# Optimization experiments

Hardware: AMD Instinct MI355X
Metric: run time of the kernel (lower is better)

## Reference

```python
import jax, jax.numpy as jnp
from jax import lax
import numpy as np

B, CIN, H, W = 1, 3, 96, 96
Q = 65536
C = 64
CU = C * 9              # feat_unfold channels
IN_DIM = CU + 2 + 2     # q_feat + rel_coord + rel_cell
HID = 256
OUT = 3
EPS_SHIFT = 1e-6


def setup_inputs():
    key = jax.random.key(0)
    ks = jax.random.split(key, 16)
    inp = jax.random.normal(ks[0], (B, CIN, H, W), jnp.float32)
    coord = jax.random.uniform(ks[1], (B, Q, 2), jnp.float32, -1.0, 1.0)
    cell = jnp.full((B, Q, 2), 2.0 / 256.0, jnp.float32)  # cell size of a 256x256 output grid
    enc_w = jax.random.normal(ks[2], (C, CIN, 3, 3), jnp.float32) * 0.1
    enc_b = jnp.zeros((C,), jnp.float32)
    dims = [IN_DIM, HID, HID, HID, HID, OUT]
    out = {"inp": inp, "coord": coord, "cell": cell, "enc_w": enc_w, "enc_b": enc_b}
    for i in range(5):
        out[f"w{i}"] = jax.random.normal(ks[3 + i], (dims[i], dims[i + 1]), jnp.float32) * (1.0 / np.sqrt(dims[i]))
        out[f"b{i}"] = jnp.zeros((dims[i + 1],), jnp.float32)
    return out


def _unfold3x3(feat):
    # F.unfold(feat, 3, padding=1).reshape(b, c*9, h, w): channel order c-major, kernel row-major
    b, c, h, w = feat.shape
    p = jnp.pad(feat, ((0, 0), (0, 0), (1, 1), (1, 1)))
    pats = jnp.stack([p[:, :, ki:ki + h, kj:kj + w] for ki in range(3) for kj in range(3)], axis=2)
    return pats.reshape(b, c * 9, h, w)


def _nearest_idx(c, n):
    # torch grid_sample nearest, align_corners=False: unnormalize then round-half-even (nearbyint)
    ix = (c + 1.0) * n / 2.0 - 0.5
    return jnp.clip(jnp.round(ix), 0, n - 1).astype(jnp.int32)


def _gather(fmap, iy, ix):
    # fmap [B,C,H,W], iy/ix [B,Q] -> [B,Q,C]
    return jax.vmap(lambda f, y, x: f[:, y, x].T)(fmap, iy, ix)


def _mlp(x, ws, bs):
    for wgt, b in zip(ws[:-1], bs[:-1]):
        x = jax.nn.relu(x @ wgt + b)
    return x @ ws[-1] + bs[-1]


def reference(inp, coord, cell, enc_w, enc_b, w0, b0, w1, b1, w2, b2, w3, b3, w4, b4):
    ws = [w0, w1, w2, w3, w4]
    bs = [b0, b1, b2, b3, b4]
    # encoder: 3x3 conv, SAME padding
    feat = lax.conv_general_dilated(inp, enc_w, (1, 1), 'SAME') + enc_b[None, :, None, None]
    feat = _unfold3x3(feat)                     # [B, C*9, H, W]
    h, w = feat.shape[2], feat.shape[3]
    rx, ry = 1.0 / h, 1.0 / w                   # 2/r/2
    # make_coord pixel centers
    fcy = -1.0 + (2.0 * jnp.arange(h, dtype=jnp.float32) + 1.0) / h   # [H]
    fcx = -1.0 + (2.0 * jnp.arange(w, dtype=jnp.float32) + 1.0) / w   # [W]
    bnd = 1.0 - 1e-6
    rel_cell = cell * jnp.array([h, w], dtype=cell.dtype)             # [B,Q,2]

    preds, areas = [], []
    for vx in (-1.0, 1.0):
        for vy in (-1.0, 1.0):
            c0 = jnp.clip(coord[..., 0] + vx * rx + EPS_SHIFT, -bnd, bnd)
            c1 = jnp.clip(coord[..., 1] + vy * ry + EPS_SHIFT, -bnd, bnd)
            iy = _nearest_idx(c0, h)            # coord[...,0] indexes dim H
            ix = _nearest_idx(c1, w)
            q_feat = _gather(feat, iy, ix)      # [B,Q,CU]
            rel0 = (coord[..., 0] - fcy[iy]) * h
            rel1 = (coord[..., 1] - fcx[ix]) * w
            mlp_in = jnp.concatenate([q_feat, rel0[..., None], rel1[..., None], rel_cell], axis=-1)
            pred = _mlp(mlp_in.reshape(-1, IN_DIM), ws, bs).reshape(coord.shape[0], coord.shape[1], OUT)
            preds.append(pred)
            areas.append(jnp.abs(rel0 * rel1) + 1e-9)

    tot_area = areas[0] + areas[1] + areas[2] + areas[3]
    # local-ensemble diagonal swap
    areas = [areas[3], areas[2], areas[1], areas[0]]
    ret = 0.0
    for pred, area in zip(preds, areas):
        ret = ret + pred * (area / tot_area)[..., None]
    return ret
```

## Files before the change

### kernel.cpp

```cpp
#include <hip/hip_runtime.h>
#include <math.h>

#define NPOS 9216

using half8  = __attribute__((ext_vector_type(8))) _Float16;
using f32x4  = __attribute__((ext_vector_type(4))) float;
using f32x16 = __attribute__((ext_vector_type(16))) float;

#define OFF_FEATT 0u
#define OFF_A0    1229312u
#define OFF_WF32  5947904u
#define OFF_WF4   6341120u
#define OFF_WB    6349312u

#define NB_FEAT 2401
#define NB_PA   768
#define NB_PW4  16
#define NB_PB   576

__global__ __launch_bounds__(256) void setup_kernel(
    const float* __restrict__ inp, const float* __restrict__ enc_w,
    const float* __restrict__ enc_b, const float* __restrict__ w0,
    const float* __restrict__ w1, const float* __restrict__ w2,
    const float* __restrict__ w3, const float* __restrict__ w4,
    _Float16* __restrict__ featT, _Float16* __restrict__ wf32,
    _Float16* __restrict__ wf4, _Float16* __restrict__ wB)
{
    int blk = blockIdx.x;
    const int t = threadIdx.x;

    if (blk < NB_FEAT) {
        int pp = blk * 4 + (t >> 6);
        int c  = t & 63;
        int py = pp / 98, px = pp - py * 98;
        float acc = 0.0f;
        if (py >= 1 && py <= 96 && px >= 1 && px <= 96) {
            int y = py - 1, x = px - 1;
            acc = enc_b[c];
            #pragma unroll
            for (int cin = 0; cin < 3; ++cin) {
                #pragma unroll
                for (int ky = 0; ky < 3; ++ky) {
                    int yy = y + ky - 1;
                    if (yy < 0 || yy >= 96) continue;
                    #pragma unroll
                    for (int kx = 0; kx < 3; ++kx) {
                        int xx = x + kx - 1;
                        if (xx < 0 || xx >= 96) continue;
                        acc = fmaf(inp[cin * NPOS + yy * 96 + xx],
                                   enc_w[c * 27 + cin * 9 + ky * 3 + kx], acc);
                    }
                }
            }
        }
        featT[pp * 64 + c] = (_Float16)acc;
        return;
    }
    blk -= NB_FEAT;
    if (blk < NB_PA) {
        int idx = blk * 256 + t;
        int l = idx >> 16;
        int r = idx & 65535;
        int j    = r & 7;
        int lane = (r >> 3) & 63;
        int nt32 = (r >> 9) & 7;
        int ks   = r >> 12;
        int n = nt32 * 32 + (lane & 31);
        int k = ks * 16 + ((lane >> 5) << 3) + j;
        const float* W = (l == 0) ? w1 : (l == 1) ? w2 : w3;
        wf32[idx] = (_Float16)W[k * 256 + n];
        return;
    }
    blk -= NB_PA;
    if (blk < NB_PW4) {
        int idx = blk * 256 + t;
        int j    = idx & 7;
        int lane = (idx >> 3) & 63;
        int ks   = idx >> 9;
        int n = lane & 15;
        int k = ks * 32 + ((lane >> 4) << 3) + j;
        wf4[idx] = (n < 3) ? (_Float16)w4[k * 3 + n] : (_Float16)0.0f;
        return;
    }
    blk -= NB_PW4;
    {
        int idx = blk * 256 + t;
        int j    = idx & 7;
        int lane = (idx >> 3) & 63;
        int ntB  = (idx >> 9) & 15;
        int ks   = (idx >> 13) & 1;
        int t9   = idx >> 14;
        int c = ks * 32 + ((lane >> 4) << 3) + j;
        int n = ntB * 16 + (lane & 15);
        wB[idx] = (_Float16)w0[(c * 9 + t9) * 256 + n];
    }
}

__global__ __launch_bounds__(256) void a0_mfma(const _Float16* __restrict__ featT,
                                               const _Float16* __restrict__ wB,
                                               const float* __restrict__ b0,
                                               _Float16* __restrict__ A0)
{
    const int lane = threadIdx.x & 63;
    const int tile = blockIdx.x * 4 + (threadIdx.x >> 6);
    const int l15  = lane & 15;
    const int l4   = lane >> 4;
    int r = tile * 16 + l15;
    int y = r / 96, x = r - y * 96;

    f32x4 acc[16];
    #pragma unroll
    for (int nt = 0; nt < 16; ++nt) acc[nt] = (f32x4){0.f, 0.f, 0.f, 0.f};

    #pragma unroll
    for (int t9 = 0; t9 < 9; ++t9) {
        int ki = t9 / 3, kj = t9 - ki * 3;
        const _Float16* ap = featT + ((y + ki) * 98 + (x + kj)) * 64 + l4 * 8;
        #pragma unroll
        for (int ks = 0; ks < 2; ++ks) {
            half8 a = *(const half8*)(ap + ks * 32);
            const _Float16* bp = wB + ((t9 * 2 + ks) * 16 * 64 + lane) * 8;
            #pragma unroll
            for (int nt = 0; nt < 16; ++nt) {
                half8 b = *(const half8*)(bp + nt * 512);
                acc[nt] = __builtin_amdgcn_mfma_f32_16x16x32_f16(a, b, acc[nt], 0, 0, 0);
            }
        }
    }
    int rb = tile * 16 + l4 * 4;
    #pragma unroll
    for (int nt = 0; nt < 16; ++nt) {
        float bb = b0[nt * 16 + l15];
        #pragma unroll
        for (int i = 0; i < 4; ++i)
            A0[(rb + i) * 256 + nt * 16 + l15] = (_Float16)(acc[nt][i] + bb);
    }
}

__device__ __forceinline__ void hidden32(_Float16 (*h)[264],
                                         const _Float16* __restrict__ W,
                                         const float* __restrict__ bias,
                                         int wm, int wn, int lane)
{
    const int l31 = lane & 31;
    const int l5  = lane >> 5;
    f32x16 a00 = {}, a01 = {}, a10 = {}, a11 = {};
    #pragma unroll
    for (int ks = 0; ks < 16; ++ks) {
        half8 Av0 = *(const half8*)&h[wm * 64 + l31][ks * 16 + l5 * 8];
        half8 Av1 = *(const half8*)&h[wm * 64 + 32 + l31][ks * 16 + l5 * 8];
        const _Float16* bp = W + (ks * 8 + wn * 2) * 512 + lane * 8;
        half8 Bv0 = *(const half8*)bp;
        half8 Bv1 = *(const half8*)(bp + 512);
        a00 = __builtin_amdgcn_mfma_f32_32x32x16_f16(Av0, Bv0, a00, 0, 0, 0);
        a01 = __builtin_amdgcn_mfma_f32_32x32x16_f16(Av0, Bv1, a01, 0, 0, 0);
        a10 = __builtin_amdgcn_mfma_f32_32x32x16_f16(Av1, Bv0, a10, 0, 0, 0);
        a11 = __builtin_amdgcn_mfma_f32_32x32x16_f16(Av1, Bv1, a11, 0, 0, 0);
    }
    __syncthreads();
    float bv0 = bias[wn * 64 + l31];
    float bv1 = bias[wn * 64 + 32 + l31];
    #pragma unroll
    for (int reg = 0; reg < 16; ++reg) {
        int rr = (reg & 3) + ((reg >> 2) << 3) + (l5 << 2);
        int r0 = wm * 64 + rr;
        int c0 = wn * 64 + l31;
        h[r0][c0]           = (_Float16)fmaxf(a00[reg] + bv0, 0.0f);
        h[r0][c0 + 32]      = (_Float16)fmaxf(a01[reg] + bv1, 0.0f);
        h[r0 + 32][c0]      = (_Float16)fmaxf(a10[reg] + bv0, 0.0f);
        h[r0 + 32][c0 + 32] = (_Float16)fmaxf(a11[reg] + bv1, 0.0f);
    }
    __syncthreads();
}

__global__ __launch_bounds__(512, 4) void fused_kernel(
    const _Float16* __restrict__ A0, const float* __restrict__ coord,
    const float* __restrict__ cell, const float* __restrict__ w0,
    const float* __restrict__ b1, const float* __restrict__ b2,
    const float* __restrict__ b3, const float* __restrict__ b4,
    const _Float16* __restrict__ wf32, const _Float16* __restrict__ wf4,
    float* __restrict__ out)
{
    __shared__ _Float16 h[128][264];
    __shared__ float pred[128][4];
    __shared__ float s_rel0[128], s_rel1[128], s_rc0[128], s_rc1[128], s_area[128];
    __shared__ int   s_pos[128];

    const int t   = threadIdx.x;
    const int blk = blockIdx.x;

    if (t < 128) {
        int r = blk * 128 + t;
        int q = r >> 2;
        int j = r & 3;
        float vx = (j & 2) ? 1.0f : -1.0f;
        float vy = (j & 1) ? 1.0f : -1.0f;
        float c0 = coord[q * 2 + 0];
        float c1 = coord[q * 2 + 1];
        const float rr  = 1.0f / 96.0f;
        const float bnd = 1.0f - 1e-6f;
        float sc0 = fminf(fmaxf(fmaf(vx, rr, c0) + 1e-6f, -bnd), bnd);
        float sc1 = fminf(fmaxf(fmaf(vy, rr, c1) + 1e-6f, -bnd), bnd);
        float fy = (sc0 + 1.0f) * 48.0f - 0.5f;
        float fx = (sc1 + 1.0f) * 48.0f - 0.5f;
        int iy = (int)rintf(fy); iy = iy < 0 ? 0 : (iy > 95 ? 95 : iy);
        int ix = (int)rintf(fx); ix = ix < 0 ? 0 : (ix > 95 ? 95 : ix);
        float fcy = -1.0f + (2.0f * (float)iy + 1.0f) / 96.0f;
        float fcx = -1.0f + (2.0f * (float)ix + 1.0f) / 96.0f;
        float rel0 = (c0 - fcy) * 96.0f;
        float rel1 = (c1 - fcx) * 96.0f;
        s_pos[t]  = iy * 96 + ix;
        s_rel0[t] = rel0;
        s_rel1[t] = rel1;
        s_rc0[t]  = cell[q * 2 + 0] * 96.0f;
        s_rc1[t]  = cell[q * 2 + 1] * 96.0f;
        s_area[t] = fabsf(rel0 * rel1) + 1e-9f;
    }
    __syncthreads();

    {
        int col = t & 255;
        int m0  = (t >> 8) * 64;
        float wa = w0[576 * 256 + col];
        float wb = w0[577 * 256 + col];
        float wc = w0[578 * 256 + col];
        float wd = w0[579 * 256 + col];
        #pragma unroll 4
        for (int mm = 0; mm < 64; ++mm) {
            int m = m0 + mm;
            float v = (float)A0[s_pos[m] * 256 + col];
            v = fmaf(s_rel0[m], wa, v);
            v = fmaf(s_rel1[m], wb, v);
            v = fmaf(s_rc0[m], wc, v);
            v = fmaf(s_rc1[m], wd, v);
            h[m][col] = (_Float16)fmaxf(v, 0.0f);
        }
    }
    __syncthreads();

    const int wave = t >> 6;
    const int lane = t & 63;
    const int wm = wave >> 2;
    const int wn = wave & 3;

    hidden32(h, wf32,             b1, wm, wn, lane);
    hidden32(h, wf32 + 65536,     b2, wm, wn, lane);
    hidden32(h, wf32 + 2 * 65536, b3, wm, wn, lane);

    {
        const int l15 = lane & 15;
        const int l4  = lane >> 4;
        f32x4 acc = (f32x4){0.f, 0.f, 0.f, 0.f};
        #pragma unroll
        for (int ks = 0; ks < 8; ++ks) {
            half8 a = *(const half8*)&h[wave * 16 + l15][ks * 32 + l4 * 8];
            half8 b = *(const half8*)&wf4[(ks * 64 + lane) * 8];
            acc = __builtin_amdgcn_mfma_f32_16x16x32_f16(a, b, acc, 0, 0, 0);
        }
        if (l15 < 3) {
            float bv = b4[l15];
            #pragma unroll
            for (int i = 0; i < 4; ++i)
                pred[wave * 16 + l4 * 4 + i][l15] = acc[i] + bv;
        }
    }
    __syncthreads();

    if (t < 96) {
        int ql = t / 3;
        int o  = t - ql * 3;
        int mb = ql * 4;
        float a0 = s_area[mb + 0];
        float a1 = s_area[mb + 1];
        float a2 = s_area[mb + 2];
        float a3 = s_area[mb + 3];
        float tot = a0 + a1 + a2 + a3;
        float rv = pred[mb + 0][o] * a3 + pred[mb + 1][o] * a2 +
                   pred[mb + 2][o] * a1 + pred[mb + 3][o] * a0;
        out[(blk * 32 + ql) * 3 + o] = rv / tot;
    }
}

extern "C" void kernel_launch(void* const* d_in, const int* in_sizes, int n_in,
                              void* d_out, int out_size, void* d_ws, size_t ws_size,
                              hipStream_t stream)
{
    (void)in_sizes; (void)n_in; (void)out_size; (void)ws_size;
    const float* inp   = (const float*)d_in[0];
    const float* coord = (const float*)d_in[1];
    const float* cell  = (const float*)d_in[2];
    const float* enc_w = (const float*)d_in[3];
    const float* enc_b = (const float*)d_in[4];
    const float* w0 = (const float*)d_in[5];
    const float* b0 = (const float*)d_in[6];
    const float* w1 = (const float*)d_in[7];
    const float* b1 = (const float*)d_in[8];
    const float* w2 = (const float*)d_in[9];
    const float* b2 = (const float*)d_in[10];
    const float* w3 = (const float*)d_in[11];
    const float* b3 = (const float*)d_in[12];
    const float* w4 = (const float*)d_in[13];
    const float* b4 = (const float*)d_in[14];
    float* outp = (float*)d_out;

    char* ws = (char*)d_ws;
    _Float16* featT = (_Float16*)(ws + OFF_FEATT);
    _Float16* A0    = (_Float16*)(ws + OFF_A0);
    _Float16* wf32  = (_Float16*)(ws + OFF_WF32);
    _Float16* wf4   = (_Float16*)(ws + OFF_WF4);
    _Float16* wB    = (_Float16*)(ws + OFF_WB);

    setup_kernel<<<dim3(NB_FEAT + NB_PA + NB_PW4 + NB_PB), dim3(256), 0, stream>>>(
        inp, enc_w, enc_b, w0, w1, w2, w3, w4, featT, wf32, wf4, wB);
    a0_mfma<<<dim3(144), dim3(256), 0, stream>>>(featT, wB, b0, A0);
    fused_kernel<<<dim3(2048), dim3(512), 0, stream>>>(A0, coord, cell, w0,
                                                       b1, b2, b3, b4, wf32, wf4, outp);
}
```

Measured before the change: 304.7 us.

## Prefetch next-layer weights across barriers and vectorize first-layer gather

Each hidden layer now preloads the first two k-slices of the next layer's weights into registers before the barrier, so the next layer's opening MFMAs do not wait on global loads. Barriers become a custom s_waitcnt lgkmcnt(0) plus s_barrier, so outstanding global loads are not drained at each sync. The first-layer gather now processes 8 columns per thread with half8 loads and float4 weight loads instead of scalar loads. This adds register pressure (eight extra half8 values) under a 512x4 launch bound, which may cause spills.

```diff
diff --git a/kernel.cpp b/kernel.cpp
--- a/kernel.cpp
+++ b/kernel.cpp
@@ -17,6 +17,10 @@
 #define NB_PA   768
 #define NB_PW4  16
 #define NB_PB   576
+
+#define BAR() do { asm volatile("s_waitcnt lgkmcnt(0)" ::: "memory"); \
+                   __builtin_amdgcn_s_barrier();                      \
+                   asm volatile("" ::: "memory"); } while (0)
 
 __global__ __launch_bounds__(256) void setup_kernel(
     const float* __restrict__ inp, const float* __restrict__ enc_w,
@@ -137,16 +141,34 @@
     }
 }
 
-__device__ __forceinline__ void hidden32(_Float16 (*h)[264],
-                                         const _Float16* __restrict__ W,
-                                         const float* __restrict__ bias,
-                                         int wm, int wn, int lane)
+__device__ __forceinline__ void hidden_layer32(
+    _Float16 (*h)[264], const _Float16* __restrict__ W,
+    const float* __restrict__ bias, const _Float16* __restrict__ Wpre,
+    bool preIsFinal,
+    half8 p0, half8 p1, half8 p2, half8 p3,
+    half8& q0, half8& q1, half8& q2, half8& q3,
+    int wm, int wn, int lane)
 {
     const int l31 = lane & 31;
     const int l5  = lane >> 5;
     f32x16 a00 = {}, a01 = {}, a10 = {}, a11 = {};
-    #pragma unroll
-    for (int ks = 0; ks < 16; ++ks) {
+
+    {
+        half8 Av0 = *(const half8*)&h[wm * 64 + l31][l5 * 8];
+        half8 Av1 = *(const half8*)&h[wm * 64 + 32 + l31][l5 * 8];
+        a00 = __builtin_amdgcn_mfma_f32_32x32x16_f16(Av0, p0, a00, 0, 0, 0);
+        a01 = __builtin_amdgcn_mfma_f32_32x32x16_f16(Av0, p1, a01, 0, 0, 0);
+        a10 = __builtin_amdgcn_mfma_f32_32x32x16_f16(Av1, p0, a10, 0, 0, 0);
+        a11 = __builtin_amdgcn_mfma_f32_32x32x16_f16(Av1, p1, a11, 0, 0, 0);
+        Av0 = *(const half8*)&h[wm * 64 + l31][16 + l5 * 8];
+        Av1 = *(const half8*)&h[wm * 64 + 32 + l31][16 + l5 * 8];
+        a00 = __builtin_amdgcn_mfma_f32_32x32x16_f16(Av0, p2, a00, 0, 0, 0);
+        a01 = __builtin_amdgcn_mfma_f32_32x32x16_f16(Av0, p3, a01, 0, 0, 0);
+        a10 = __builtin_amdgcn_mfma_f32_32x32x16_f16(Av1, p2, a10, 0, 0, 0);
+        a11 = __builtin_amdgcn_mfma_f32_32x32x16_f16(Av1, p3, a11, 0, 0, 0);
+    }
+    #pragma unroll
+    for (int ks = 2; ks < 16; ++ks) {
         half8 Av0 = *(const half8*)&h[wm * 64 + l31][ks * 16 + l5 * 8];
         half8 Av1 = *(const half8*)&h[wm * 64 + 32 + l31][ks * 16 + l5 * 8];
         const _Float16* bp = W + (ks * 8 + wn * 2) * 512 + lane * 8;
@@ -157,7 +179,22 @@
         a10 = __builtin_amdgcn_mfma_f32_32x32x16_f16(Av1, Bv0, a10, 0, 0, 0);
         a11 = __builtin_amdgcn_mfma_f32_32x32x16_f16(Av1, Bv1, a11, 0, 0, 0);
     }
-    __syncthreads();
+
+    if (preIsFinal) {
+        q0 = *(const half8*)&Wpre[(0 * 64 + lane) * 8];
+        q1 = *(const half8*)&Wpre[(1 * 64 + lane) * 8];
+        q2 = *(const half8*)&Wpre[(2 * 64 + lane) * 8];
+        q3 = *(const half8*)&Wpre[(3 * 64 + lane) * 8];
+    } else {
+        const _Float16* bp0 = Wpre + (wn * 2) * 512 + lane * 8;
+        const _Float16* bp1 = Wpre + (8 + wn * 2) * 512 + lane * 8;
+        q0 = *(const half8*)bp0;
+        q1 = *(const half8*)(bp0 + 512);
+        q2 = *(const half8*)bp1;
+        q3 = *(const half8*)(bp1 + 512);
+    }
+
+    BAR();
     float bv0 = bias[wn * 64 + l31];
     float bv1 = bias[wn * 64 + 32 + l31];
     #pragma unroll
@@ -170,7 +207,7 @@
         h[r0 + 32][c0]      = (_Float16)fmaxf(a10[reg] + bv0, 0.0f);
         h[r0 + 32][c0 + 32] = (_Float16)fmaxf(a11[reg] + bv1, 0.0f);
     }
-    __syncthreads();
+    BAR();
 }
 
 __global__ __launch_bounds__(512, 4) void fused_kernel(
@@ -219,41 +256,72 @@
     __syncthreads();
 
     {
-        int col = t & 255;
-        int m0  = (t >> 8) * 64;
-        float wa = w0[576 * 256 + col];
-        float wb = w0[577 * 256 + col];
-        float wc = w0[578 * 256 + col];
-        float wd = w0[579 * 256 + col];
-        #pragma unroll 4
-        for (int mm = 0; mm < 64; ++mm) {
-            int m = m0 + mm;
-            float v = (float)A0[s_pos[m] * 256 + col];
-            v = fmaf(s_rel0[m], wa, v);
-            v = fmaf(s_rel1[m], wb, v);
-            v = fmaf(s_rc0[m], wc, v);
-            v = fmaf(s_rc1[m], wd, v);
-            h[m][col] = (_Float16)fmaxf(v, 0.0f);
-        }
-    }
-    __syncthreads();
+        const int cg = t & 31;
+        const int rg = t >> 5;
+        const float* wbase = w0 + 576 * 256 + cg * 8;
+        float4 wa0 = *(const float4*)(wbase);
+        float4 wa1 = *(const float4*)(wbase + 4);
+        float4 wb0 = *(const float4*)(wbase + 256);
+        float4 wb1 = *(const float4*)(wbase + 260);
+        float4 wc0 = *(const float4*)(wbase + 512);
+        float4 wc1 = *(const float4*)(wbase + 516);
+        float4 wd0 = *(const float4*)(wbase + 768);
+        float4 wd1 = *(const float4*)(wbase + 772);
+        #pragma unroll
+        for (int rr = 0; rr < 8; ++rr) {
+            const int m = rg * 8 + rr;
+            half8 qv = *(const half8*)&A0[s_pos[m] * 256 + cg * 8];
+            float r0 = s_rel0[m], r1 = s_rel1[m], rc0 = s_rc0[m], rc1 = s_rc1[m];
+            half8 o;
+            float v;
+            v = (float)qv[0]; v = fmaf(r0,wa0.x,v); v = fmaf(r1,wb0.x,v); v = fmaf(rc0,wc0.x,v); v = fmaf(rc1,wd0.x,v); o[0] = (_Float16)fmaxf(v,0.f);
+            v = (float)qv[1]; v = fmaf(r0,wa0.y,v); v = fmaf(r1,wb0.y,v); v = fmaf(rc0,wc0.y,v); v = fmaf(rc1,wd0.y,v); o[1] = (_Float16)fmaxf(v,0.f);
+            v = (float)qv[2]; v = fmaf(r0,wa0.z,v); v = fmaf(r1,wb0.z,v); v = fmaf(rc0,wc0.z,v); v = fmaf(rc1,wd0.z,v); o[2] = (_Float16)fmaxf(v,0.f);
+            v = (float)qv[3]; v = fmaf(r0,wa0.w,v); v = fmaf(r1,wb0.w,v); v = fmaf(rc0,wc0.w,v); v = fmaf(rc1,wd0.w,v); o[3] = (_Float16)fmaxf(v,0.f);
+            v = (float)qv[4]; v = fmaf(r0,wa1.x,v); v = fmaf(r1,wb1.x,v); v = fmaf(rc0,wc1.x,v); v = fmaf(rc1,wd1.x,v); o[4] = (_Float16)fmaxf(v,0.f);
+            v = (float)qv[5]; v = fmaf(r0,wa1.y,v); v = fmaf(r1,wb1.y,v); v = fmaf(rc0,wc1.y,v); v = fmaf(rc1,wd1.y,v); o[5] = (_Float16)fmaxf(v,0.f);
+            v = (float)qv[6]; v = fmaf(r0,wa1.z,v); v = fmaf(r1,wb1.z,v); v = fmaf(rc0,wc1.z,v); v = fmaf(rc1,wd1.z,v); o[6] = (_Float16)fmaxf(v,0.f);
+            v = (float)qv[7]; v = fmaf(r0,wa1.w,v); v = fmaf(r1,wb1.w,v); v = fmaf(rc0,wc1.w,v); v = fmaf(rc1,wd1.w,v); o[7] = (_Float16)fmaxf(v,0.f);
+            *(half8*)&h[m][cg * 8] = o;
+        }
+    }
 
     const int wave = t >> 6;
     const int lane = t & 63;
     const int wm = wave >> 2;
     const int wn = wave & 3;
 
-    hidden32(h, wf32,             b1, wm, wn, lane);
-    hidden32(h, wf32 + 65536,     b2, wm, wn, lane);
-    hidden32(h, wf32 + 2 * 65536, b3, wm, wn, lane);
+    half8 p0, p1, p2, p3, q0, q1, q2, q3;
+    {
+        const _Float16* bp0 = wf32 + (wn * 2) * 512 + lane * 8;
+        const _Float16* bp1 = wf32 + (8 + wn * 2) * 512 + lane * 8;
+        p0 = *(const half8*)bp0;
+        p1 = *(const half8*)(bp0 + 512);
+        p2 = *(const half8*)bp1;
+        p3 = *(const half8*)(bp1 + 512);
+    }
+    BAR();
+
+    hidden_layer32(h, wf32,             b1, wf32 + 65536,     false, p0,p1,p2,p3, q0,q1,q2,q3, wm, wn, lane);
+    hidden_layer32(h, wf32 + 65536,     b2, wf32 + 2 * 65536, false, q0,q1,q2,q3, p0,p1,p2,p3, wm, wn, lane);
+    hidden_layer32(h, wf32 + 2 * 65536, b3, wf4,              true,  p0,p1,p2,p3, q0,q1,q2,q3, wm, wn, lane);
 
     {
         const int l15 = lane & 15;
         const int l4  = lane >> 4;
         f32x4 acc = (f32x4){0.f, 0.f, 0.f, 0.f};
+        half8 a;
+        a = *(const half8*)&h[wave * 16 + l15][0 * 32 + l4 * 8];
+        acc = __builtin_amdgcn_mfma_f32_16x16x32_f16(a, q0, acc, 0, 0, 0);
+        a = *(const half8*)&h[wave * 16 + l15][1 * 32 + l4 * 8];
+        acc = __builtin_amdgcn_mfma_f32_16x16x32_f16(a, q1, acc, 0, 0, 0);
+        a = *(const half8*)&h[wave * 16 + l15][2 * 32 + l4 * 8];
+        acc = __builtin_amdgcn_mfma_f32_16x16x32_f16(a, q2, acc, 0, 0, 0);
+        a = *(const half8*)&h[wave * 16 + l15][3 * 32 + l4 * 8];
+        acc = __builtin_amdgcn_mfma_f32_16x16x32_f16(a, q3, acc, 0, 0, 0);
         #pragma unroll
-        for (int ks = 0; ks < 8; ++ks) {
-            half8 a = *(const half8*)&h[wave * 16 + l15][ks * 32 + l4 * 8];
+        for (int ks = 4; ks < 8; ++ks) {
+            a = *(const half8*)&h[wave * 16 + l15][ks * 32 + l4 * 8];
             half8 b = *(const half8*)&wf4[(ks * 64 + lane) * 8];
             acc = __builtin_amdgcn_mfma_f32_16x16x32_f16(a, b, acc, 0, 0, 0);
         }
@@ -264,7 +332,7 @@
                 pred[wave * 16 + l4 * 4 + i][l15] = acc[i] + bv;
         }
     }
-    __syncthreads();
+    BAR();
 
     if (t < 96) {
         int ql = t / 3;
```

Measured after the change: 297.0 us. -2.5%, faster.
